# Kernel optimization log

Hardware: AMD Instinct MI355X
Metric: run time of the kernel (lower is better)

Reference implementation:

```python
import jax, jax.numpy as jnp
import numpy as np

DIM = 256
WIN = 8          # window height == width
HEADS = 8
HEAD_DIM = DIM // HEADS
NW = 64          # number of windows per image
B_IMG = 16
N = WIN * WIN    # 64 tokens per window
B_ = B_IMG * NW  # 1024


def _relative_position_index():
    # matches torch.meshgrid default (ij) indexing
    coords = np.stack(np.meshgrid(np.arange(WIN), np.arange(WIN), indexing='ij'))  # [2,Wh,Ww]
    flat = coords.reshape(2, -1)                                # [2,N]
    rel = flat[:, :, None] - flat[:, None, :]                   # [2,N,N]
    rel = rel.transpose(1, 2, 0).copy()                         # [N,N,2]
    rel[:, :, 0] += WIN - 1
    rel[:, :, 1] += WIN - 1
    rel[:, :, 0] *= 2 * WIN - 1
    return rel.sum(-1).astype(np.int32)                         # [N,N]


def setup_inputs() -> dict:
    key = jax.random.key(0)
    ks = jax.random.split(key, 24)
    std = 0.02

    def lin(i):
        W = jax.random.normal(ks[i], (DIM, DIM), jnp.float32) * std
        b = jax.random.normal(ks[i + 1], (DIM,), jnp.float32) * std
        return W, b

    Wq, bq = lin(0)
    Wk, bk = lin(2)
    Wv, bv = lin(4)
    Wvs, bvs = lin(6)      # v_scale
    Wvh, bvh = lin(8)      # v_shift
    Wpx, bpx = lin(10)     # proj_x
    Wps, bps = lin(12)     # proj_scale
    Wph, bph = lin(14)     # proj_shift

    bias_table = jax.random.normal(ks[16], ((2 * WIN - 1) * (2 * WIN - 1), HEADS), jnp.float32) * std
    rel_idx = jnp.asarray(_relative_position_index())

    q_input = jax.random.normal(ks[17], (B_, N, DIM), jnp.float32)
    k_input = jax.random.normal(ks[18], (B_, N, DIM), jnp.float32)
    v_input = jax.random.normal(ks[19], (B_, N, DIM), jnp.float32)
    scale_in = jax.random.normal(ks[20], (B_, N, DIM), jnp.float32)
    shift_in = jax.random.normal(ks[21], (B_, N, DIM), jnp.float32)

    # shifted-window style mask: 0 where attendable, large negative otherwise
    u = jax.random.uniform(ks[22], (NW, N, N), jnp.float32)
    mask = jnp.where(u < 0.15, -100.0, 0.0).astype(jnp.float32)

    return {
        'q_input': q_input, 'k_input': k_input, 'v_input': v_input,
        'scale_in': scale_in, 'shift_in': shift_in, 'mask': mask,
        'Wq': Wq, 'bq': bq, 'Wk': Wk, 'bk': bk, 'Wv': Wv, 'bv': bv,
        'Wvs': Wvs, 'bvs': bvs, 'Wvh': Wvh, 'bvh': bvh,
        'Wpx': Wpx, 'bpx': bpx, 'Wps': Wps, 'bps': bps, 'Wph': Wph, 'bph': bph,
        'bias_table': bias_table, 'rel_idx': rel_idx,
    }


def reference(q_input, k_input, v_input, scale_in, shift_in, mask,
              Wq, bq, Wk, bk, Wv, bv, Wvs, bvs, Wvh, bvh,
              Wpx, bpx, Wps, bps, Wph, bph, bias_table, rel_idx):
    B, Ntok, C = q_input.shape
    scale = HEAD_DIM ** -0.5

    def to_heads(x, W, b):
        # nn.Linear: x @ W.T + b, then split heads -> [B, H, N, hd]
        return (x @ W.T + b).reshape(B, Ntok, HEADS, HEAD_DIM).transpose(0, 2, 1, 3)

    q = to_heads(q_input, Wq, bq) * scale
    k = to_heads(k_input, Wk, bk)
    v = to_heads(v_input, Wv, bv)
    v_scale = to_heads(scale_in, Wvs, bvs)
    v_shift = to_heads(shift_in, Wvh, bvh)

    attn = jnp.einsum('bhnd,bhmd->bhnm', q, k)                    # [B,H,N,N]
    rel_bias = bias_table[rel_idx]                                # [N,N,H] gather
    attn = attn + rel_bias.transpose(2, 0, 1)[None]               # add per-head bias

    nW = mask.shape[0]
    attn = attn.reshape(B // nW, nW, HEADS, Ntok, Ntok) + mask[None, :, None]
    attn = jax.nn.softmax(attn.reshape(B, HEADS, Ntok, Ntok), axis=-1)

    def out_proj(val, Wp, bp):
        o = jnp.einsum('bhnm,bhmd->bhnd', attn, val)
        o = o.transpose(0, 2, 1, 3).reshape(B, Ntok, C)
        return o @ Wp.T + bp

    x_out = out_proj(v, Wpx, bpx)
    scale_out = out_proj(v_scale, Wps, bps)
    shift_out = out_proj(v_shift, Wph, bph)
    return (x_out, scale_out, shift_out)
```

## Files before the change

kernel.cpp:

```cpp
#include <hip/hip_runtime.h>


typedef __attribute__((ext_vector_type(8))) __bf16 bf16x8;
typedef __attribute__((ext_vector_type(4))) float f32x4;
typedef __attribute__((ext_vector_type(4))) unsigned short u16x4;

__device__ __forceinline__ unsigned short f2bf(float f) {
  return __builtin_bit_cast(unsigned short, (__bf16)f);
}
__device__ __forceinline__ unsigned pk2(float lo, float hi) {
  return (unsigned)f2bf(lo) | ((unsigned)f2bf(hi) << 16);
}
__device__ __forceinline__ int swz256(int row, int col) {
  return row * 256 + (col ^ ((row & 31) << 3));
}
__device__ __forceinline__ f32x4 mfma16(bf16x8 a, bf16x8 b, f32x4 c) {
  return __builtin_amdgcn_mfma_f32_16x16x32_bf16(a, b, c, 0, 0, 0);
}

__global__ void pack_weights(const float* __restrict__ W0, const float* __restrict__ W1,
                             const float* __restrict__ W2, const float* __restrict__ W3,
                             const float* __restrict__ W4, const float* __restrict__ W5,
                             const float* __restrict__ W6, const float* __restrict__ W7,
                             unsigned short* __restrict__ pk) {
  int t = blockIdx.x * 256 + threadIdx.x;
  int mat = t >> 13;
  int w   = (t >> 11) & 3;
  int blk = (t >> 9) & 3;
  int kc  = (t >> 6) & 7;
  int l   = t & 63;
  const float* W = (mat == 0) ? W0 : (mat == 1) ? W1 : (mat == 2) ? W2 : (mat == 3) ? W3
                 : (mat == 4) ? W4 : (mat == 5) ? W5 : (mat == 6) ? W6 : W7;
  const float* src = W + (64 * w + 16 * blk + (l & 15)) * 256 + 32 * kc + 8 * (l >> 4);
  unsigned short* dst = pk + (size_t)t * 8;
#pragma unroll
  for (int i = 0; i < 8; ++i) dst[i] = f2bf(src[i]);
}

__global__ void make_bmt(const float* __restrict__ mask, const float* __restrict__ btab,
                         const int* __restrict__ ridx, float* __restrict__ bmt) {
  int t = blockIdx.x * 256 + threadIdx.x;
  int r  = t & 3;
  int l  = (t >> 2) & 63;
  int mf = (t >> 8) & 3;
  int nf = (t >> 10) & 3;
  int h  = (t >> 12) & 7;
  int wi = t >> 15;
  int q = 16 * nf + (l & 15);
  int k = 16 * mf + 4 * (l >> 4) + r;
  bmt[t] = mask[(wi * 64 + q) * 64 + k] + btab[ridx[q * 64 + k] * 8 + h];
}

__device__ __forceinline__ bf16x8 butterfly(f32x4 C0, f32x4 C1, int c4, int r16) {
  unsigned a0 = pk2(C0[0], C0[1]), a1 = pk2(C0[2], C0[3]);
  unsigned b0 = pk2(C1[0], C1[1]), b1 = pk2(C1[2], C1[3]);
  int src0 = (((2 * c4) & 3) << 4) + r16;
  int src1 = (((2 * c4 + 1) & 3) << 4) + r16;
  unsigned A0 = (unsigned)__shfl((int)a0, src0);
  unsigned A1 = (unsigned)__shfl((int)a1, src0);
  unsigned A2 = (unsigned)__shfl((int)a0, src1);
  unsigned A3 = (unsigned)__shfl((int)a1, src1);
  unsigned B0 = (unsigned)__shfl((int)b0, src0);
  unsigned B1 = (unsigned)__shfl((int)b1, src0);
  unsigned B2 = (unsigned)__shfl((int)b0, src1);
  unsigned B3 = (unsigned)__shfl((int)b1, src1);
  bool hi = c4 >= 2;
  union { unsigned u[4]; bf16x8 v; } r;
  r.u[0] = hi ? B0 : A0;
  r.u[1] = hi ? B1 : A1;
  r.u[2] = hi ? B2 : A2;
  r.u[3] = hi ? B3 : A3;
  return r.v;
}

__device__ __forceinline__ void load_tile(f32x4 r[8], const float* __restrict__ X,
                                          int b, int tid) {
  const f32x4* src = reinterpret_cast<const f32x4*>(X + (size_t)b * 16384);
#pragma unroll
  for (int it = 0; it < 8; ++it) r[it] = src[it * 512 + tid];
}
__device__ __forceinline__ void write_tile(unsigned short* T, const f32x4 r[8], int tid) {
#pragma unroll
  for (int it = 0; it < 8; ++it) {
    int f = it * 512 + tid;
    int row = f >> 6;
    int col = (f & 63) << 2;
    u16x4 p;
    p[0] = f2bf(r[it][0]); p[1] = f2bf(r[it][1]);
    p[2] = f2bf(r[it][2]); p[3] = f2bf(r[it][3]);
    *reinterpret_cast<u16x4*>(T + swz256(row, col)) = p;
  }
}

__device__ __forceinline__ const unsigned short* pwBase(const unsigned short* pk,
                                                        int mat, int w) {
  return pk + mat * 65536 + (w >> 1) * 16384 + (w & 1) * 8192;
}

__device__ __forceinline__ void projT_head(const unsigned short* __restrict__ T,
                                           const unsigned short* __restrict__ pw,
                                           const float* __restrict__ bias, float scale,
                                           int lane, int w, bf16x8 frag[4]) {
  const int r16 = lane & 15, c4 = lane >> 4;
  f32x4 z = {0.f, 0.f, 0.f, 0.f};
  f32x4 acc[2][4];
#pragma unroll
  for (int j = 0; j < 2; ++j)
#pragma unroll
    for (int nf = 0; nf < 4; ++nf) acc[j][nf] = z;
#pragma unroll
  for (int kc = 0; kc < 8; ++kc) {
    bf16x8 aw[2], bx[4];
#pragma unroll
    for (int j = 0; j < 2; ++j)
      aw[j] = *reinterpret_cast<const bf16x8*>(pw + j * 4096 + kc * 512 + lane * 8);
#pragma unroll
    for (int nf = 0; nf < 4; ++nf)
      bx[nf] = *reinterpret_cast<const bf16x8*>(T + swz256(16 * nf + r16, 32 * kc + 8 * c4));
#pragma unroll
    for (int j = 0; j < 2; ++j)
#pragma unroll
      for (int nf = 0; nf < 4; ++nf) acc[j][nf] = mfma16(aw[j], bx[nf], acc[j][nf]);
  }
#pragma unroll
  for (int j = 0; j < 2; ++j) {
    f32x4 b4 = *reinterpret_cast<const f32x4*>(bias + 32 * w + 16 * j + 4 * c4);
#pragma unroll
    for (int nf = 0; nf < 4; ++nf)
#pragma unroll
      for (int r = 0; r < 4; ++r) acc[j][nf][r] = (acc[j][nf][r] + b4[r]) * scale;
  }
#pragma unroll
  for (int nf = 0; nf < 4; ++nf)
    frag[nf] = butterfly(acc[0][nf], acc[1][nf], c4, r16);
}

__device__ __forceinline__ void attn_head(const bf16x8 Qf[4], const bf16x8 Kf[4],
                                          const float* __restrict__ bmb,
                                          int lane, bf16x8 Pf[4][2]) {
  const int r16 = lane & 15, c4 = lane >> 4;
  f32x4 z = {0.f, 0.f, 0.f, 0.f};
#pragma unroll
  for (int qb = 0; qb < 4; ++qb) {
    f32x4 s[4];
#pragma unroll
    for (int t = 0; t < 4; ++t) s[t] = mfma16(Kf[t], Qf[qb], z);
    float mx = -1e30f;
#pragma unroll
    for (int t = 0; t < 4; ++t) {
      f32x4 bm4 = *reinterpret_cast<const f32x4*>(bmb + (((qb * 4 + t) * 64 + lane) << 2));
#pragma unroll
      for (int r = 0; r < 4; ++r) {
        s[t][r] += bm4[r];
        mx = fmaxf(mx, s[t][r]);
      }
    }
    mx = fmaxf(mx, __shfl_xor(mx, 16));
    mx = fmaxf(mx, __shfl_xor(mx, 32));
    float sum = 0.f;
#pragma unroll
    for (int t = 0; t < 4; ++t)
#pragma unroll
      for (int r = 0; r < 4; ++r) {
        s[t][r] = __expf(s[t][r] - mx);
        sum += s[t][r];
      }
    sum += __shfl_xor(sum, 16);
    sum += __shfl_xor(sum, 32);
    float inv = 1.0f / sum;
#pragma unroll
    for (int kc = 0; kc < 2; ++kc) {
      f32x4 p0, p1;
#pragma unroll
      for (int r = 0; r < 4; ++r) {
        p0[r] = s[2 * kc][r] * inv;
        p1[r] = s[2 * kc + 1][r] * inv;
      }
      Pf[qb][kc] = butterfly(p0, p1, c4, r16);
    }
  }
}

__device__ __forceinline__ void projN32(const unsigned short* __restrict__ T,
                                        const unsigned short* __restrict__ pw,
                                        int lane, f32x4 acc[4][2]) {
  const int r16 = lane & 15, c4 = lane >> 4;
  f32x4 z = {0.f, 0.f, 0.f, 0.f};
#pragma unroll
  for (int mf = 0; mf < 4; ++mf)
#pragma unroll
    for (int nf = 0; nf < 2; ++nf) acc[mf][nf] = z;
#pragma unroll
  for (int kc = 0; kc < 8; ++kc) {
    bf16x8 a[4], bb[2];
#pragma unroll
    for (int mf = 0; mf < 4; ++mf)
      a[mf] = *reinterpret_cast<const bf16x8*>(T + swz256(16 * mf + r16, 32 * kc + 8 * c4));
#pragma unroll
    for (int nf = 0; nf < 2; ++nf)
      bb[nf] = *reinterpret_cast<const bf16x8*>(pw + nf * 4096 + kc * 512 + lane * 8);
#pragma unroll
    for (int mf = 0; mf < 4; ++mf)
#pragma unroll
      for (int nf = 0; nf < 2; ++nf) acc[mf][nf] = mfma16(a[mf], bb[nf], acc[mf][nf]);
  }
}

__device__ __forceinline__ void vFrag(f32x4 acc[4][2], const float* __restrict__ bias,
                                      int lane, int w, bf16x8 Vf[2][2]) {
  const int r16 = lane & 15, c4 = lane >> 4;
#pragma unroll
  for (int nf = 0; nf < 2; ++nf) {
    float bb = bias[32 * w + 16 * nf + r16];
#pragma unroll
    for (int mf = 0; mf < 4; ++mf)
#pragma unroll
      for (int r = 0; r < 4; ++r) acc[mf][nf][r] += bb;
  }
#pragma unroll
  for (int nf = 0; nf < 2; ++nf) {
    Vf[0][nf] = butterfly(acc[0][nf], acc[1][nf], c4, r16);
    Vf[1][nf] = butterfly(acc[2][nf], acc[3][nf], c4, r16);
  }
}

__device__ __forceinline__ void pv_store(const bf16x8 Pf[4][2], const bf16x8 Vf[2][2],
                                         unsigned short* OS, int lane, int w) {
  const int r16 = lane & 15, c4 = lane >> 4;
  f32x4 z = {0.f, 0.f, 0.f, 0.f};
  f32x4 o[4][2];
#pragma unroll
  for (int qb = 0; qb < 4; ++qb)
#pragma unroll
    for (int nf = 0; nf < 2; ++nf) o[qb][nf] = z;
#pragma unroll
  for (int kc = 0; kc < 2; ++kc)
#pragma unroll
    for (int qb = 0; qb < 4; ++qb)
#pragma unroll
      for (int nf = 0; nf < 2; ++nf)
        o[qb][nf] = mfma16(Pf[qb][kc], Vf[kc][nf], o[qb][nf]);
#pragma unroll
  for (int qb = 0; qb < 4; ++qb)
#pragma unroll
    for (int nf = 0; nf < 2; ++nf)
#pragma unroll
      for (int r = 0; r < 4; ++r)
        OS[swz256(16 * qb + 4 * c4 + r, 32 * w + 16 * nf + r16)] = f2bf(o[qb][nf][r]);
}

__device__ __forceinline__ void outProj(const unsigned short* __restrict__ OS,
                                        const unsigned short* __restrict__ pw,
                                        const float* __restrict__ bias,
                                        float* __restrict__ dst, int lane, int w) {
  const int r16 = lane & 15, c4 = lane >> 4;
  f32x4 acc[4][2];
  projN32(OS, pw, lane, acc);
#pragma unroll
  for (int nf = 0; nf < 2; ++nf) {
    float bb = bias[32 * w + 16 * nf + r16];
#pragma unroll
    for (int mf = 0; mf < 4; ++mf)
#pragma unroll
      for (int r = 0; r < 4; ++r)
        dst[(16 * mf + 4 * c4 + r) * 256 + 32 * w + 16 * nf + r16] = acc[mf][nf][r] + bb;
  }
}

__global__ __launch_bounds__(512, 2) void win_attn(
    const float* __restrict__ gq, const float* __restrict__ gk, const float* __restrict__ gv,
    const float* __restrict__ gsc, const float* __restrict__ gsh,
    const unsigned short* __restrict__ pk,
    const float* __restrict__ b_q, const float* __restrict__ b_k, const float* __restrict__ b_v,
    const float* __restrict__ b_vs, const float* __restrict__ b_vh,
    const float* __restrict__ b_px, const float* __restrict__ b_ps, const float* __restrict__ b_ph,
    const float* __restrict__ bmt, float* __restrict__ out) {
  __shared__ __align__(16) unsigned short sm[81920];
  unsigned short* T0 = sm;
  unsigned short* T1 = sm + 16384;
  unsigned short* T2 = sm + 32768;
  unsigned short* T3 = sm + 49152;
  unsigned short* T4 = sm + 65536;

  const int b    = blockIdx.x;
  const int tid  = threadIdx.x;
  const int lane = tid & 63;
  const int w    = tid >> 6;
  const int wi   = b & 63;

  bf16x8 Qf[4], Kf[4], Pf[4][2], Vf[2][2];

  {
    f32x4 rA[8], rB[8];
    load_tile(rA, gq, b, tid);
    load_tile(rB, gk, b, tid);
    write_tile(T0, rA, tid);
    write_tile(T1, rB, tid);
  }
  __syncthreads();

  {
    f32x4 rA[8];
    load_tile(rA, gv, b, tid);
    projT_head(T0, pwBase(pk, 0, w), b_q, 0.17677669529663687f, lane, w, Qf);
    projT_head(T1, pwBase(pk, 1, w), b_k, 1.0f, lane, w, Kf);
    attn_head(Qf, Kf, bmt + ((size_t)(wi * 8 + w) << 12), lane, Pf);
    write_tile(T2, rA, tid);
  }
  __syncthreads();

  {
    f32x4 rA[8], rB[8];
    load_tile(rA, gsc, b, tid);
    load_tile(rB, gsh, b, tid);
    {
      f32x4 acc[4][2];
      projN32(T2, pwBase(pk, 2, w), lane, acc);
      vFrag(acc, b_v, lane, w, Vf);
    }
    pv_store(Pf, Vf, T0, lane, w);
    write_tile(T3, rA, tid);
    write_tile(T4, rB, tid);
  }
  __syncthreads();

  outProj(T0, pwBase(pk, 5, w), b_px, out + (size_t)b * 16384, lane, w);
  {
    f32x4 acc[4][2];
    projN32(T3, pwBase(pk, 3, w), lane, acc);
    vFrag(acc, b_vs, lane, w, Vf);
  }
  pv_store(Pf, Vf, T1, lane, w);
  __syncthreads();

  outProj(T1, pwBase(pk, 6, w), b_ps, out + 16777216 + (size_t)b * 16384, lane, w);
  {
    f32x4 acc[4][2];
    projN32(T4, pwBase(pk, 4, w), lane, acc);
    vFrag(acc, b_vh, lane, w, Vf);
  }
  pv_store(Pf, Vf, T2, lane, w);
  __syncthreads();

  outProj(T2, pwBase(pk, 7, w), b_ph, out + 33554432 + (size_t)b * 16384, lane, w);
}

extern "C" void kernel_launch(void* const* d_in, const int* in_sizes, int n_in,
                              void* d_out, int out_size, void* d_ws, size_t ws_size,
                              hipStream_t stream) {
  const float* Xq   = (const float*)d_in[0];
  const float* Xk   = (const float*)d_in[1];
  const float* Xv   = (const float*)d_in[2];
  const float* Xsc  = (const float*)d_in[3];
  const float* Xsh  = (const float*)d_in[4];
  const float* mask = (const float*)d_in[5];
  const float* Wq   = (const float*)d_in[6];  const float* bq  = (const float*)d_in[7];
  const float* Wk   = (const float*)d_in[8];  const float* bk  = (const float*)d_in[9];
  const float* Wv   = (const float*)d_in[10]; const float* bv  = (const float*)d_in[11];
  const float* Wvs  = (const float*)d_in[12]; const float* bvs = (const float*)d_in[13];
  const float* Wvh  = (const float*)d_in[14]; const float* bvh = (const float*)d_in[15];
  const float* Wpx  = (const float*)d_in[16]; const float* bpx = (const float*)d_in[17];
  const float* Wps  = (const float*)d_in[18]; const float* bps = (const float*)d_in[19];
  const float* Wph  = (const float*)d_in[20]; const float* bph = (const float*)d_in[21];
  const float* btab = (const float*)d_in[22];
  const int*   ridx = (const int*)d_in[23];

  unsigned short* pk = (unsigned short*)d_ws;
  float* bmt = (float*)((char*)d_ws + (size_t)8 * 65536 * 2);

  pack_weights<<<256, 256, 0, stream>>>(Wq, Wk, Wv, Wvs, Wvh, Wpx, Wps, Wph, pk);
  make_bmt<<<8192, 256, 0, stream>>>(mask, btab, ridx, bmt);
  win_attn<<<1024, 512, 0, stream>>>(Xq, Xk, Xv, Xsc, Xsh, pk,
                                     bq, bk, bv, bvs, bvh, bpx, bps, bph,
                                     bmt, (float*)d_out);
}
```

Baseline: 215.0 us.

## Raise MFMA wave priority, vectorize output stores via shuffles, defer shift tile load

Wraps each MFMA loop in s_setprio(1)/s_setprio(0) so waves issuing matrix work get scheduling priority over waves doing loads or softmax. The output projection now transposes results across lanes with shuffles so each lane writes a 16-byte vector instead of scattered scalar stores. The shift-input tile load moves one stage later so it overlaps the x output projection and lowers peak register pressure. The shuffles add extra cross-lane instructions, and the shift-tile write now happens in the same stage as the scale-path compute.

Result: slower. 252.7 us (+17.5%).

```diff
diff --git a/kernel.cpp b/kernel.cpp
--- a/kernel.cpp
+++ b/kernel.cpp
@@ -108,6 +108,7 @@
   for (int j = 0; j < 2; ++j)
 #pragma unroll
     for (int nf = 0; nf < 4; ++nf) acc[j][nf] = z;
+  __builtin_amdgcn_s_setprio(1);
 #pragma unroll
   for (int kc = 0; kc < 8; ++kc) {
     bf16x8 aw[2], bx[4];
@@ -122,6 +123,7 @@
 #pragma unroll
       for (int nf = 0; nf < 4; ++nf) acc[j][nf] = mfma16(aw[j], bx[nf], acc[j][nf]);
   }
+  __builtin_amdgcn_s_setprio(0);
 #pragma unroll
   for (int j = 0; j < 2; ++j) {
     f32x4 b4 = *reinterpret_cast<const f32x4*>(bias + 32 * w + 16 * j + 4 * c4);
@@ -143,8 +145,10 @@
 #pragma unroll
   for (int qb = 0; qb < 4; ++qb) {
     f32x4 s[4];
+    __builtin_amdgcn_s_setprio(1);
 #pragma unroll
     for (int t = 0; t < 4; ++t) s[t] = mfma16(Kf[t], Qf[qb], z);
+    __builtin_amdgcn_s_setprio(0);
     float mx = -1e30f;
 #pragma unroll
     for (int t = 0; t < 4; ++t) {
@@ -190,6 +194,7 @@
   for (int mf = 0; mf < 4; ++mf)
 #pragma unroll
     for (int nf = 0; nf < 2; ++nf) acc[mf][nf] = z;
+  __builtin_amdgcn_s_setprio(1);
 #pragma unroll
   for (int kc = 0; kc < 8; ++kc) {
     bf16x8 a[4], bb[2];
@@ -204,6 +209,7 @@
 #pragma unroll
       for (int nf = 0; nf < 2; ++nf) acc[mf][nf] = mfma16(a[mf], bb[nf], acc[mf][nf]);
   }
+  __builtin_amdgcn_s_setprio(0);
 }
 
 __device__ __forceinline__ void vFrag(f32x4 acc[4][2], const float* __restrict__ bias,
@@ -233,6 +239,7 @@
   for (int qb = 0; qb < 4; ++qb)
 #pragma unroll
     for (int nf = 0; nf < 2; ++nf) o[qb][nf] = z;
+  __builtin_amdgcn_s_setprio(1);
 #pragma unroll
   for (int kc = 0; kc < 2; ++kc)
 #pragma unroll
@@ -240,6 +247,7 @@
 #pragma unroll
       for (int nf = 0; nf < 2; ++nf)
         o[qb][nf] = mfma16(Pf[qb][kc], Vf[kc][nf], o[qb][nf]);
+  __builtin_amdgcn_s_setprio(0);
 #pragma unroll
   for (int qb = 0; qb < 4; ++qb)
 #pragma unroll
@@ -256,15 +264,27 @@
   const int r16 = lane & 15, c4 = lane >> 4;
   f32x4 acc[4][2];
   projN32(OS, pw, lane, acc);
-#pragma unroll
-  for (int nf = 0; nf < 2; ++nf) {
-    float bb = bias[32 * w + 16 * nf + r16];
-#pragma unroll
-    for (int mf = 0; mf < 4; ++mf)
-#pragma unroll
-      for (int r = 0; r < 4; ++r)
-        dst[(16 * mf + 4 * c4 + r) * 256 + 32 * w + 16 * nf + r16] = acc[mf][nf][r] + bb;
-  }
+  const int rsel = r16 & 3;
+  const int sbase = ((r16 >> 2) << 4) + 4 * c4;
+#pragma unroll
+  for (int mf = 0; mf < 4; ++mf)
+#pragma unroll
+    for (int nf = 0; nf < 2; ++nf) {
+      float bb = bias[32 * w + 16 * nf + r16];
+      f32x4 a;
+#pragma unroll
+      for (int r = 0; r < 4; ++r) a[r] = acc[mf][nf][r] + bb;
+      f32x4 v;
+#pragma unroll
+      for (int j = 0; j < 4; ++j) {
+        float t0 = __shfl(a[0], sbase + j);
+        float t1 = __shfl(a[1], sbase + j);
+        float t2 = __shfl(a[2], sbase + j);
+        float t3 = __shfl(a[3], sbase + j);
+        v[j] = (rsel == 0) ? t0 : (rsel == 1) ? t1 : (rsel == 2) ? t2 : t3;
+      }
+      *reinterpret_cast<f32x4*>(dst + (16 * mf + r16) * 256 + 32 * w + 16 * nf + 4 * c4) = v;
+    }
 }
 
 __global__ __launch_bounds__(512, 2) void win_attn(
@@ -310,9 +330,8 @@
   __syncthreads();
 
   {
-    f32x4 rA[8], rB[8];
+    f32x4 rA[8];
     load_tile(rA, gsc, b, tid);
-    load_tile(rB, gsh, b, tid);
     {
       f32x4 acc[4][2];
       projN32(T2, pwBase(pk, 2, w), lane, acc);
@@ -320,17 +339,21 @@
     }
     pv_store(Pf, Vf, T0, lane, w);
     write_tile(T3, rA, tid);
-    write_tile(T4, rB, tid);
-  }
-  __syncthreads();
-
-  outProj(T0, pwBase(pk, 5, w), b_px, out + (size_t)b * 16384, lane, w);
-  {
-    f32x4 acc[4][2];
-    projN32(T3, pwBase(pk, 3, w), lane, acc);
-    vFrag(acc, b_vs, lane, w, Vf);
-  }
-  pv_store(Pf, Vf, T1, lane, w);
+  }
+  __syncthreads();
+
+  {
+    f32x4 rA[8];
+    load_tile(rA, gsh, b, tid);
+    outProj(T0, pwBase(pk, 5, w), b_px, out + (size_t)b * 16384, lane, w);
+    {
+      f32x4 acc[4][2];
+      projN32(T3, pwBase(pk, 3, w), lane, acc);
+      vFrag(acc, b_vs, lane, w, Vf);
+    }
+    pv_store(Pf, Vf, T1, lane, w);
+    write_tile(T4, rA, tid);
+  }
   __syncthreads();
 
   outProj(T1, pwBase(pk, 6, w), b_ps, out + 16777216 + (size_t)b * 16384, lane, w);
```
